# Kernel tuning notes

Measured on AMD Instinct MI355X. Metric: run time of the kernel, lower is better.

Reference implementation:

```python
import jax, jax.numpy as jnp
import numpy as np

BATCH = 2048
INPUT_DIM = 256
NUM_SUBCARRIERS = 256
HIDDEN_DIM = 256


def setup_inputs() -> dict:
    key = jax.random.key(0)
    ks = jax.random.split(key, 7)
    C, I, H = NUM_SUBCARRIERS, INPUT_DIM, HIDDEN_DIM
    # PyTorch nn.Linear default init: U(-1/sqrt(fan_in), 1/sqrt(fan_in))
    s1 = 1.0 / np.sqrt(I)
    s2 = 1.0 / np.sqrt(H)
    x = jax.random.normal(ks[0], (BATCH, I), dtype=jnp.float32)
    W1 = jax.random.uniform(ks[1], (C, I, H), jnp.float32, -s1, s1)
    b1 = jax.random.uniform(ks[2], (C, H), jnp.float32, -s1, s1)
    W2 = jax.random.uniform(ks[3], (C, H, H), jnp.float32, -s2, s2)
    b2 = jax.random.uniform(ks[4], (C, H), jnp.float32, -s2, s2)
    W3 = jax.random.uniform(ks[5], (C, H), jnp.float32, -s2, s2)  # [C, H] (out dim 1 squeezed)
    b3 = jax.random.uniform(ks[6], (C,), jnp.float32, -s2, s2)
    return {"x": x, "W1": W1, "b1": b1, "W2": W2, "b2": b2, "W3": W3, "b3": b3}


def reference(x, W1, b1, W2, b2, W3, b3):
    # Stacked (batched) version of the per-subcarrier Python loop:
    # for each subcarrier c: relu(relu(x @ W1[c] + b1[c]) @ W2[c] + b2[c]) @ W3[c] + b3[c]
    h1 = jax.nn.relu(jnp.einsum('bi,cih->cbh', x, W1) + b1[:, None, :])   # [C, B, H]
    h2 = jax.nn.relu(jnp.einsum('cbh,chk->cbk', h1, W2) + b2[:, None, :])  # [C, B, H]
    out = jnp.einsum('cbh,ch->cb', h2, W3) + b3[:, None]                   # [C, B]
    return out.T  # [B, C], matches torch.cat(outputs, dim=1)
```

## Files before the change

kernel.cpp:

```cpp
#include <hip/hip_runtime.h>

typedef unsigned short u16;
using u16x4  = __attribute__((ext_vector_type(4))) unsigned short;
using u16x8  = __attribute__((ext_vector_type(8))) unsigned short;
using bf16x8 = __attribute__((ext_vector_type(8))) short;
using f32x4  = __attribute__((ext_vector_type(4))) float;

__device__ __forceinline__ u16 f2bf(float f) {
  union { float f; unsigned u; } v; v.f = f;
  unsigned r = v.u + 0x7FFFu + ((v.u >> 16) & 1u);
  return (u16)(r >> 16);
}

__global__ void convert_x_k(const float* __restrict__ in, u16* __restrict__ out) {
  int i = blockIdx.x * 256 + threadIdx.x;
  float4 v = ((const float4*)in)[i];
  u16x4 u;
  u.x = f2bf(v.x); u.y = f2bf(v.y); u.z = f2bf(v.z); u.w = f2bf(v.w);
  ((u16x4*)out)[i] = u;
}

__global__ __launch_bounds__(256) void transpose_w2_k(
    const float* __restrict__ W1, const float* __restrict__ W2,
    u16* __restrict__ w1t, u16* __restrict__ w2t) {
  __shared__ float tile[64][65];
  const int bid = blockIdx.x;
  const int mat = bid >> 4;
  const int tl  = bid & 15;
  const int i0 = (tl >> 2) * 64, h0 = (tl & 3) * 64;
  const float* src = (mat < 256) ? (W1 + mat * 65536) : (W2 + (mat - 256) * 65536);
  u16*       dst   = (mat < 256) ? (w1t + mat * 65536) : (w2t + (mat - 256) * 65536);
  const int t = threadIdx.x;
#pragma unroll
  for (int j = 0; j < 4; ++j) {
    int lin = j * 256 + t;
    int row = lin >> 4, c4 = lin & 15;
    float4 v = *(const float4*)(src + (i0 + row) * 256 + h0 + c4 * 4);
    tile[row][c4 * 4 + 0] = v.x; tile[row][c4 * 4 + 1] = v.y;
    tile[row][c4 * 4 + 2] = v.z; tile[row][c4 * 4 + 3] = v.w;
  }
  __syncthreads();
  const int col = t >> 2;
  const int kk  = (t & 3) * 8;
#pragma unroll
  for (int p = 0; p < 2; ++p) {
    u16x8 o;
#pragma unroll
    for (int jj = 0; jj < 8; ++jj)
      o[jj] = f2bf(tile[p * 32 + kk + jj][col]);
    *(u16x8*)(dst + ((i0 >> 5) + p) * 8192 + (h0 + col) * 32 + kk) = o;
  }
}

__global__ __launch_bounds__(512, 4) void rf_main_k(
    const u16* __restrict__ xb, const u16* __restrict__ w1t, const u16* __restrict__ w2t,
    const float* __restrict__ b1, const float* __restrict__ b2,
    const float* __restrict__ w3, const float* __restrict__ b3,
    float* __restrict__ out) {
  __shared__ u16 sH[128 * 264];
  __shared__ float red[512];

  const int bid  = blockIdx.x;
  const int xcd  = bid & 7;
  const int j8   = bid >> 3;
  const int c    = xcd * 32 + (j8 >> 4);
  const int b0   = (j8 & 15) * 128;
  const int t    = threadIdx.x;
  const int lane = t & 63;
  const int w    = t >> 6;
  const int l15  = lane & 15;
  const int quad = lane >> 4;
  const int half = w >> 2;
  const int nw   = (w & 3) * 64;

  const u16* w1c = w1t + c * 65536;
  const u16* w2c = w2t + c * 65536;
  const int boff  = (nw + l15) * 32 + quad * 8;
  const int abase = (half * 64 + l15) * 264 + quad * 8;

  f32x4  acc[4][4] = {};
  bf16x8 bA[4], bB[4];

#define LOADB(dst, base)                                        \
  { _Pragma("unroll")                                           \
    for (int _n = 0; _n < 4; ++_n)                              \
      dst[_n] = *(const bf16x8*)((base) + _n * 512); }

#define COMPUTE(bfr, ch)                                        \
  { _Pragma("unroll")                                           \
    for (int _m = 0; _m < 4; ++_m) {                            \
      bf16x8 _a = *(const bf16x8*)&sH[abase + _m * (16*264) + (ch) * 32]; \
      _Pragma("unroll")                                         \
      for (int _n = 0; _n < 4; ++_n)                            \
        acc[_m][_n] = __builtin_amdgcn_mfma_f32_16x16x32_bf16(_a, bfr[_n], acc[_m][_n], 0, 0, 0); \
    } }

  LOADB(bA, w1c + boff);

#pragma unroll
  for (int i = 0; i < 8; ++i) {
    int flat = i * 512 + t;
    int r = flat >> 5, s = flat & 31;
    u16x8 g = *(const u16x8*)(xb + (b0 + r) * 256 + s * 8);
    *(u16x8*)&sH[r * 264 + s * 8] = g;
  }
  __syncthreads();

#pragma unroll 1
  for (int ch = 0; ch < 8; ch += 2) {
    LOADB(bB, w1c + (ch + 1) * 8192 + boff);
    COMPUTE(bA, ch);
    const u16* nxt = (ch == 6) ? (w2c + boff)
                               : (w1c + (ch + 2) * 8192 + boff);
    LOADB(bA, nxt);
    COMPUTE(bB, ch + 1);
  }

  __syncthreads();
#pragma unroll
  for (int ni = 0; ni < 4; ++ni) {
    int col = nw + ni * 16 + l15;
    float bias = b1[c * 256 + col];
#pragma unroll
    for (int mi = 0; mi < 4; ++mi)
#pragma unroll
      for (int r = 0; r < 4; ++r) {
        int row = half * 64 + mi * 16 + quad * 4 + r;
        float v = acc[mi][ni][r] + bias;
        v = v > 0.f ? v : 0.f;
        sH[row * 264 + col] = f2bf(v);
        acc[mi][ni][r] = 0.f;
      }
  }
  __syncthreads();

#pragma unroll 1
  for (int ch = 0; ch < 8; ch += 2) {
    LOADB(bB, w2c + (ch + 1) * 8192 + boff);
    COMPUTE(bA, ch);
    if (ch < 6) LOADB(bA, w2c + (ch + 2) * 8192 + boff);
    COMPUTE(bB, ch + 1);
  }

  float part[16];
#pragma unroll
  for (int i = 0; i < 16; ++i) part[i] = 0.f;
#pragma unroll
  for (int ni = 0; ni < 4; ++ni) {
    int col = nw + ni * 16 + l15;
    float bias = b2[c * 256 + col];
    float w3v  = w3[c * 256 + col];
#pragma unroll
    for (int mi = 0; mi < 4; ++mi)
#pragma unroll
      for (int r = 0; r < 4; ++r) {
        float v = acc[mi][ni][r] + bias;
        v = v > 0.f ? v : 0.f;
        part[mi * 4 + r] += v * w3v;
      }
  }
#pragma unroll
  for (int m = 1; m < 16; m <<= 1)
#pragma unroll
    for (int i = 0; i < 16; ++i)
      part[i] += __shfl_xor(part[i], m, 64);

  if (l15 == 0) {
#pragma unroll
    for (int mi = 0; mi < 4; ++mi)
#pragma unroll
      for (int r = 0; r < 4; ++r)
        red[w * 64 + mi * 16 + quad * 4 + r] = part[mi * 4 + r];
  }
  __syncthreads();
  if (t < 128) {
    int hr = t >> 6, rr = t & 63;
    float v = red[(hr * 4 + 0) * 64 + rr] + red[(hr * 4 + 1) * 64 + rr] +
              red[(hr * 4 + 2) * 64 + rr] + red[(hr * 4 + 3) * 64 + rr] + b3[c];
    out[(b0 + t) * 256 + c] = v;
  }
#undef LOADB
#undef COMPUTE
}

extern "C" void kernel_launch(void* const* d_in, const int* in_sizes, int n_in,
                              void* d_out, int out_size, void* d_ws, size_t ws_size,
                              hipStream_t stream) {
  const float* x  = (const float*)d_in[0];
  const float* W1 = (const float*)d_in[1];
  const float* b1 = (const float*)d_in[2];
  const float* W2 = (const float*)d_in[3];
  const float* b2 = (const float*)d_in[4];
  const float* W3 = (const float*)d_in[5];
  const float* b3 = (const float*)d_in[6];
  float* out = (float*)d_out;

  char* ws = (char*)d_ws;
  u16* xb  = (u16*)ws;
  u16* w1t = (u16*)(ws + (1u << 20));
  u16* w2t = (u16*)(ws + (1u << 20) + (32u << 20));

  convert_x_k   <<<512,  256, 0, stream>>>(x,  xb);
  transpose_w2_k<<<8192, 256, 0, stream>>>(W1, W2, w1t, w2t);
  rf_main_k     <<<4096, 512, 0, stream>>>(xb, w1t, w2t, b1, b2, W3, b3, out);
}
```

Measured before the change: 316.1 us.

## Switch main GEMMs to 32x32x16 MFMA with transposed operand roles

Restructures the fused MLP kernel to use 32x32x16 bf16 MFMA instead of 16x16x32. Weights become the A operand and hidden activations from LDS the B operand, so each wave computes a transposed 64x64 tile. The weight pre-transpose is changed to a 16-wide k-chunk layout to match. Biases are folded into the accumulator initialisation, packed bf16 conversion is used for the hidden write-back, and the final reduction drops the shuffle-xor tree for a small LDS sum. The goal is fewer MFMA instructions and fewer LDS reads per FLOP, at the cost of a new data layout and different register pressure.

```diff
diff --git a/kernel.cpp b/kernel.cpp
--- a/kernel.cpp
+++ b/kernel.cpp
@@ -5,11 +5,18 @@
 using u16x8  = __attribute__((ext_vector_type(8))) unsigned short;
 using bf16x8 = __attribute__((ext_vector_type(8))) short;
 using f32x4  = __attribute__((ext_vector_type(4))) float;
+using f32x16 = __attribute__((ext_vector_type(16))) float;
 
 __device__ __forceinline__ u16 f2bf(float f) {
   union { float f; unsigned u; } v; v.f = f;
   unsigned r = v.u + 0x7FFFu + ((v.u >> 16) & 1u);
   return (u16)(r >> 16);
+}
+
+__device__ __forceinline__ unsigned cvt_pk_bf16(float a, float b) {
+  unsigned d;
+  asm("v_cvt_pk_bf16_f32 %0, %1, %2" : "=v"(d) : "v"(a), "v"(b));
+  return d;
 }
 
 __global__ void convert_x_k(const float* __restrict__ in, u16* __restrict__ out) {
@@ -48,7 +55,7 @@
 #pragma unroll
     for (int jj = 0; jj < 8; ++jj)
       o[jj] = f2bf(tile[p * 32 + kk + jj][col]);
-    *(u16x8*)(dst + ((i0 >> 5) + p) * 8192 + (h0 + col) * 32 + kk) = o;
+    *(u16x8*)(dst + ((i0 >> 4) + 2 * p + (kk >> 4)) * 4096 + (h0 + col) * 16 + (kk & 8)) = o;
   }
 }
 
@@ -58,7 +65,7 @@
     const float* __restrict__ w3, const float* __restrict__ b3,
     float* __restrict__ out) {
   __shared__ u16 sH[128 * 264];
-  __shared__ float red[512];
+  __shared__ float red[8 * 128];
 
   const int bid  = blockIdx.x;
   const int xcd  = bid & 7;
@@ -68,34 +75,50 @@
   const int t    = threadIdx.x;
   const int lane = t & 63;
   const int w    = t >> 6;
-  const int l15  = lane & 15;
-  const int quad = lane >> 4;
-  const int half = w >> 2;
-  const int nw   = (w & 3) * 64;
+  const int l31  = lane & 31;
+  const int hi   = lane >> 5;
+  const bool hiH = hi != 0;
+  const int wq   = w & 3;
+  const int bh   = w >> 2;
+  const int m_base = wq * 64;
+  const int n_base = bh * 64;
 
   const u16* w1c = w1t + c * 65536;
   const u16* w2c = w2t + c * 65536;
-  const int boff  = (nw + l15) * 32 + quad * 8;
-  const int abase = (half * 64 + l15) * 264 + quad * 8;
-
-  f32x4  acc[4][4] = {};
-  bf16x8 bA[4], bB[4];
-
-#define LOADB(dst, base)                                        \
-  { _Pragma("unroll")                                           \
-    for (int _n = 0; _n < 4; ++_n)                              \
-      dst[_n] = *(const bf16x8*)((base) + _n * 512); }
-
-#define COMPUTE(bfr, ch)                                        \
-  { _Pragma("unroll")                                           \
-    for (int _m = 0; _m < 4; ++_m) {                            \
-      bf16x8 _a = *(const bf16x8*)&sH[abase + _m * (16*264) + (ch) * 32]; \
-      _Pragma("unroll")                                         \
-      for (int _n = 0; _n < 4; ++_n)                            \
-        acc[_m][_n] = __builtin_amdgcn_mfma_f32_16x16x32_bf16(_a, bfr[_n], acc[_m][_n], 0, 0, 0); \
-    } }
-
-  LOADB(bA, w1c + boff);
+  const int aoff = (m_base + l31) * 16 + hi * 8;
+  const int bbase = (n_base + l31) * 264 + hi * 8;
+  const int bidx = __builtin_amdgcn_readfirstlane(c * 256 + m_base);
+
+  f32x16 acc[2][2];
+  bf16x8 aA[2], aB[2];
+
+#define LOADA(dst, base)                                         \
+  { dst[0] = *(const bf16x8*)(base);                             \
+    dst[1] = *(const bf16x8*)((base) + 512); }
+
+#define COMPUTE(fr, ch)                                          \
+  { bf16x8 _b0 = *(const bf16x8*)&sH[bbase + (ch) * 16];         \
+    bf16x8 _b1 = *(const bf16x8*)&sH[bbase + (ch) * 16 + 8448];  \
+    acc[0][0] = __builtin_amdgcn_mfma_f32_32x32x16_bf16(fr[0], _b0, acc[0][0], 0, 0, 0); \
+    acc[1][0] = __builtin_amdgcn_mfma_f32_32x32x16_bf16(fr[1], _b0, acc[1][0], 0, 0, 0); \
+    acc[0][1] = __builtin_amdgcn_mfma_f32_32x32x16_bf16(fr[0], _b1, acc[0][1], 0, 0, 0); \
+    acc[1][1] = __builtin_amdgcn_mfma_f32_32x32x16_bf16(fr[1], _b1, acc[1][1], 0, 0, 0); }
+
+#define INIT_ACC(bp)                                             \
+  { _Pragma("unroll")                                            \
+    for (int _mi = 0; _mi < 2; ++_mi) {                          \
+      _Pragma("unroll")                                          \
+      for (int _g = 0; _g < 4; ++_g) {                           \
+        f32x4 _lo = *(const f32x4*)((bp) + bidx + _mi * 32 + _g * 8);     \
+        f32x4 _h4 = *(const f32x4*)((bp) + bidx + _mi * 32 + _g * 8 + 4); \
+        _Pragma("unroll")                                        \
+        for (int _r = 0; _r < 4; ++_r) {                         \
+          float _v = hiH ? _h4[_r] : _lo[_r];                    \
+          acc[_mi][0][_g * 4 + _r] = _v;                         \
+          acc[_mi][1][_g * 4 + _r] = _v;                         \
+        } } } }
+
+  LOADA(aA, w1c + aoff);
 
 #pragma unroll
   for (int i = 0; i < 8; ++i) {
@@ -104,83 +127,74 @@
     u16x8 g = *(const u16x8*)(xb + (b0 + r) * 256 + s * 8);
     *(u16x8*)&sH[r * 264 + s * 8] = g;
   }
+  INIT_ACC(b1);
   __syncthreads();
 
 #pragma unroll 1
-  for (int ch = 0; ch < 8; ch += 2) {
-    LOADB(bB, w1c + (ch + 1) * 8192 + boff);
-    COMPUTE(bA, ch);
-    const u16* nxt = (ch == 6) ? (w2c + boff)
-                               : (w1c + (ch + 2) * 8192 + boff);
-    LOADB(bA, nxt);
-    COMPUTE(bB, ch + 1);
-  }
-
-  __syncthreads();
-#pragma unroll
-  for (int ni = 0; ni < 4; ++ni) {
-    int col = nw + ni * 16 + l15;
-    float bias = b1[c * 256 + col];
-#pragma unroll
-    for (int mi = 0; mi < 4; ++mi)
+  for (int ch = 0; ch < 16; ch += 2) {
+    LOADA(aB, w1c + (ch + 1) * 4096 + aoff);
+    COMPUTE(aA, ch);
+    const u16* nxt = (ch == 14) ? (w2c + aoff)
+                                : (w1c + (ch + 2) * 4096 + aoff);
+    LOADA(aA, nxt);
+    COMPUTE(aB, ch + 1);
+  }
+
+  __syncthreads();
+#pragma unroll
+  for (int mi = 0; mi < 2; ++mi)
+#pragma unroll
+    for (int nj = 0; nj < 2; ++nj) {
+      const int row = n_base + nj * 32 + l31;
+#pragma unroll
+      for (int g = 0; g < 4; ++g) {
+        float v0 = fmaxf(acc[mi][nj][g * 4 + 0], 0.f);
+        float v1 = fmaxf(acc[mi][nj][g * 4 + 1], 0.f);
+        float v2 = fmaxf(acc[mi][nj][g * 4 + 2], 0.f);
+        float v3 = fmaxf(acc[mi][nj][g * 4 + 3], 0.f);
+        uint2 p;
+        p.x = cvt_pk_bf16(v0, v1);
+        p.y = cvt_pk_bf16(v2, v3);
+        *(uint2*)&sH[row * 264 + m_base + mi * 32 + g * 8 + 4 * hi] = p;
+      }
+    }
+  INIT_ACC(b2);
+  __syncthreads();
+
+#pragma unroll 1
+  for (int ch = 0; ch < 16; ch += 2) {
+    LOADA(aB, w2c + (ch + 1) * 4096 + aoff);
+    COMPUTE(aA, ch);
+    if (ch < 14) LOADA(aA, w2c + (ch + 2) * 4096 + aoff);
+    COMPUTE(aB, ch + 1);
+  }
+
+  float part0 = 0.f, part1 = 0.f;
+#pragma unroll
+  for (int mi = 0; mi < 2; ++mi)
+#pragma unroll
+    for (int g = 0; g < 4; ++g) {
+      f32x4 wlo = *(const f32x4*)(w3 + bidx + mi * 32 + g * 8);
+      f32x4 whi = *(const f32x4*)(w3 + bidx + mi * 32 + g * 8 + 4);
 #pragma unroll
       for (int r = 0; r < 4; ++r) {
-        int row = half * 64 + mi * 16 + quad * 4 + r;
-        float v = acc[mi][ni][r] + bias;
-        v = v > 0.f ? v : 0.f;
-        sH[row * 264 + col] = f2bf(v);
-        acc[mi][ni][r] = 0.f;
+        float wv = hiH ? whi[r] : wlo[r];
+        part0 += fmaxf(acc[mi][0][g * 4 + r], 0.f) * wv;
+        part1 += fmaxf(acc[mi][1][g * 4 + r], 0.f) * wv;
       }
-  }
-  __syncthreads();
-
-#pragma unroll 1
-  for (int ch = 0; ch < 8; ch += 2) {
-    LOADB(bB, w2c + (ch + 1) * 8192 + boff);
-    COMPUTE(bA, ch);
-    if (ch < 6) LOADB(bA, w2c + (ch + 2) * 8192 + boff);
-    COMPUTE(bB, ch + 1);
-  }
-
-  float part[16];
-#pragma unroll
-  for (int i = 0; i < 16; ++i) part[i] = 0.f;
-#pragma unroll
-  for (int ni = 0; ni < 4; ++ni) {
-    int col = nw + ni * 16 + l15;
-    float bias = b2[c * 256 + col];
-    float w3v  = w3[c * 256 + col];
-#pragma unroll
-    for (int mi = 0; mi < 4; ++mi)
-#pragma unroll
-      for (int r = 0; r < 4; ++r) {
-        float v = acc[mi][ni][r] + bias;
-        v = v > 0.f ? v : 0.f;
-        part[mi * 4 + r] += v * w3v;
-      }
-  }
-#pragma unroll
-  for (int m = 1; m < 16; m <<= 1)
-#pragma unroll
-    for (int i = 0; i < 16; ++i)
-      part[i] += __shfl_xor(part[i], m, 64);
-
-  if (l15 == 0) {
-#pragma unroll
-    for (int mi = 0; mi < 4; ++mi)
-#pragma unroll
-      for (int r = 0; r < 4; ++r)
-        red[w * 64 + mi * 16 + quad * 4 + r] = part[mi * 4 + r];
-  }
+    }
+  red[(wq * 2 + hi) * 128 + n_base + l31]      = part0;
+  red[(wq * 2 + hi) * 128 + n_base + 32 + l31] = part1;
   __syncthreads();
   if (t < 128) {
-    int hr = t >> 6, rr = t & 63;
-    float v = red[(hr * 4 + 0) * 64 + rr] + red[(hr * 4 + 1) * 64 + rr] +
-              red[(hr * 4 + 2) * 64 + rr] + red[(hr * 4 + 3) * 64 + rr] + b3[c];
+    float v = b3[c];
+#pragma unroll
+    for (int k = 0; k < 8; ++k) v += red[k * 128 + t];
     out[(b0 + t) * 256 + c] = v;
   }
-#undef LOADB
+#undef LOADA
 #undef COMPUTE
+#undef INIT_ACC
 }
 
 extern "C" void kernel_launch(void* const* d_in, const int* in_sizes, int n_in,
```

Result: faster. 304.3 us (-3.8%).
